# Optimization experiments

Measured on AMD Instinct MI355X. Metric: run time of the kernel, lower is better.

Reference implementation:

```python
import jax, jax.numpy as jnp
import numpy as np

V, L, H, D, S, B = 32000, 6, 16, 1024, 512, 4
DK = D // H
DF = 4 * D
EPS = 1e-5


def setup_inputs() -> dict:
    key = jax.random.key(0)
    ks = jax.random.split(key, 24)
    std = 0.02
    def w(k, shape):
        return jax.random.normal(k, shape, dtype=jnp.float32) * std
    inp = {
        'x': jax.random.randint(ks[0], (B, S), 0, V),
        'tok_emb': w(ks[1], (V, D)),
        # per-layer params stacked on leading L axis; Linear stored as [in,out]
        'wq': w(ks[2], (L, D, D)), 'bq': jnp.zeros((L, D)),
        'wk': w(ks[3], (L, D, D)), 'bk': jnp.zeros((L, D)),
        'wv': w(ks[4], (L, D, D)), 'bv': jnp.zeros((L, D)),
        'wo': w(ks[5], (L, D, D)), 'bo': jnp.zeros((L, D)),
        'ln1_g': jnp.ones((L, D)), 'ln1_b': jnp.zeros((L, D)),
        'w1': w(ks[6], (L, D, DF)), 'b1': jnp.zeros((L, DF)),
        'w2': w(ks[7], (L, DF, D)), 'b2': jnp.zeros((L, D)),
        'ln2_g': jnp.ones((L, D)), 'ln2_b': jnp.zeros((L, D)),
        'lnf_g': jnp.ones((D,)), 'lnf_b': jnp.zeros((D,)),
        'lm_w': w(ks[8], (D, V)),
    }
    return inp


def _layernorm(x, g, b):
    mu = jnp.mean(x, axis=-1, keepdims=True)
    var = jnp.mean(jnp.square(x - mu), axis=-1, keepdims=True)
    return (x - mu) * jax.lax.rsqrt(var + EPS) * g + b


def _sinusoidal_pe(seq_len, d_model):
    pos = jnp.arange(seq_len, dtype=jnp.float32)[:, None]
    div = jnp.exp(jnp.arange(0, d_model, 2, dtype=jnp.float32) * (-np.log(10000.0) / d_model))
    pe = jnp.zeros((seq_len, d_model), dtype=jnp.float32)
    pe = pe.at[:, 0::2].set(jnp.sin(pos * div))
    pe = pe.at[:, 1::2].set(jnp.cos(pos * div))
    return pe  # [S, D]


def _gpt_forward(x, tok_emb, wq, bq, wk, bk, wv, bv, wo, bo,
                 ln1_g, ln1_b, w1, b1, w2, b2, ln2_g, ln2_b,
                 lnf_g, lnf_b, lm_w):
    b, s = x.shape
    h = tok_emb[x] + _sinusoidal_pe(s, D)  # [B,S,D]
    causal = jnp.tril(jnp.ones((s, s), dtype=bool))  # True = keep
    scale = 1.0 / np.sqrt(DK)

    def block(h, p):
        (wq, bq, wk, bk, wv, bv, wo, bo,
         ln1_g, ln1_b, w1, b1, w2, b2, ln2_g, ln2_b) = p
        hn = _layernorm(h, ln1_g, ln1_b)
        q = (hn @ wq + bq).reshape(b, s, H, DK)
        k = (hn @ wk + bk).reshape(b, s, H, DK)
        v = (hn @ wv + bv).reshape(b, s, H, DK)
        scores = jnp.einsum('bqhd,bkhd->bhqk', q, k) * scale
        scores = jnp.where(causal, scores, -1e9)
        attn = jax.nn.softmax(scores, axis=-1)
        ctx = jnp.einsum('bhqk,bkhd->bqhd', attn, v).reshape(b, s, D)
        h = h + (ctx @ wo + bo)
        hn2 = _layernorm(h, ln2_g, ln2_b)
        ff = jax.nn.gelu(hn2 @ w1 + b1, approximate=False) @ w2 + b2
        return h + ff, None

    params = (wq, bq, wk, bk, wv, bv, wo, bo,
              ln1_g, ln1_b, w1, b1, w2, b2, ln2_g, ln2_b)
    h, _ = jax.lax.scan(block, h, params)
    h = _layernorm(h, lnf_g, lnf_b)
    return h @ lm_w  # [B,S,V] logits


def reference(x, tok_emb, wq, bq, wk, bk, wv, bv, wo, bo,
              ln1_g, ln1_b, w1, b1, w2, b2, ln2_g, ln2_b,
              lnf_g, lnf_b, lm_w):
    return _gpt_forward(x, tok_emb, wq, bq, wk, bk, wv, bv, wo, bo,
                        ln1_g, ln1_b, w1, b1, w2, b2, ln2_g, ln2_b,
                        lnf_g, lnf_b, lm_w)
```

## Files before the change

### kernel.cpp

```cpp
#include <hip/hip_runtime.h>
#include <hip/hip_bf16.h>
#include <math.h>

#define V_SIZE 32000
#define L_NUM 6
#define H_NUM 16
#define D_MODEL 1024
#define S_LEN 512
#define B_SZ 4
#define DF_DIM 4096
#define ROWS (B_SZ * S_LEN)
#define QKV_N (3 * D_MODEL)
#define KVBLK 64

typedef unsigned short u16;
typedef __attribute__((ext_vector_type(8))) short short8v;
typedef __attribute__((ext_vector_type(4))) float f32x4;

__device__ __forceinline__ float b2f(u16 b) {
  union { float f; unsigned u; } c; c.u = ((unsigned)b) << 16; return c.f;
}
__device__ __forceinline__ u16 f2b(float f) {
  __hip_bfloat16 h = __float2bfloat16(f);
  union { __hip_bfloat16 h; u16 u; } c; c.h = h; return c.u;
}
__device__ __forceinline__ void g2l16(const void* g, void* l) {
  __builtin_amdgcn_global_load_lds(
      (const __attribute__((address_space(1))) void*)g,
      (__attribute__((address_space(3))) void*)l, 16, 0, 0);
}

__global__ __launch_bounds__(256) void embed_kernel(
    const int* __restrict__ x, const float* __restrict__ tok_emb,
    float* __restrict__ h) {
  int row = blockIdx.x;
  int s = row % S_LEN;
  int tok = x[row];
  const float* te = tok_emb + (size_t)tok * D_MODEL;
  float* hr = h + (size_t)row * D_MODEL;
  float pos = (float)s;
  const float c = 9.210340371976184f / (float)D_MODEL;
#pragma unroll
  for (int i = 0; i < D_MODEL / 256; ++i) {
    int d = threadIdx.x + i * 256;
    float freq = expf(-(float)(d & ~1) * c);
    float ang = pos * freq;
    float pe = (d & 1) ? cosf(ang) : sinf(ang);
    hr[d] = te[d] + pe;
  }
}

__global__ __launch_bounds__(256) void layernorm_kernel(
    const float* __restrict__ in, const float* __restrict__ g,
    const float* __restrict__ b, u16* __restrict__ out) {
  const int row = blockIdx.x * 4 + (threadIdx.x >> 6);
  const int lane = threadIdx.x & 63;
  const float4* xr = (const float4*)(in + (size_t)row * D_MODEL);
  float4 v[4];
  float s1 = 0.f, s2 = 0.f;
#pragma unroll
  for (int i = 0; i < 4; ++i) {
    float4 t = xr[lane + i * 64];
    v[i] = t;
    s1 += t.x + t.y + t.z + t.w;
    s2 += t.x * t.x + t.y * t.y + t.z * t.z + t.w * t.w;
  }
#pragma unroll
  for (int off = 32; off; off >>= 1) {
    s1 += __shfl_xor(s1, off, 64);
    s2 += __shfl_xor(s2, off, 64);
  }
  const float mu = s1 * (1.0f / D_MODEL);
  const float var = s2 * (1.0f / D_MODEL) - mu * mu;
  const float rstd = rsqrtf(var + 1e-5f);
  u16* orow = out + (size_t)row * D_MODEL;
#pragma unroll
  for (int i = 0; i < 4; ++i) {
    const int d = (lane + i * 64) * 4;
    const float4 gv = *(const float4*)&g[d];
    const float4 bv = *(const float4*)&b[d];
    u16 o0 = f2b((v[i].x - mu) * rstd * gv.x + bv.x);
    u16 o1 = f2b((v[i].y - mu) * rstd * gv.y + bv.y);
    u16 o2 = f2b((v[i].z - mu) * rstd * gv.z + bv.z);
    u16 o3 = f2b((v[i].w - mu) * rstd * gv.w + bv.w);
    uint2 pk;
    pk.x = (unsigned)o0 | ((unsigned)o1 << 16);
    pk.y = (unsigned)o2 | ((unsigned)o3 << 16);
    *(uint2*)&orow[d] = pk;
  }
}

__global__ __launch_bounds__(256) void transpose_cvt(
    const float* __restrict__ W, u16* __restrict__ Wt, int K, int N,
    long out_stride) {
  __shared__ float t[64][33];
  const float* Wl = W + (size_t)blockIdx.z * K * N;
  u16* Wtl = Wt + (size_t)blockIdx.z * out_stride;
  const int n0 = blockIdx.x * 32, k0 = blockIdx.y * 64;
  const int tx = threadIdx.x & 31, ty = threadIdx.x >> 5;
#pragma unroll
  for (int i = 0; i < 64; i += 8)
    t[ty + i][tx] = Wl[(size_t)(k0 + ty + i) * N + n0 + tx];
  __syncthreads();
#pragma unroll
  for (int j = 0; j < 32; j += 8) {
    const int n = ty + j;
    u16 lo = f2b(t[2 * tx][n]);
    u16 hi = f2b(t[2 * tx + 1][n]);
    *(unsigned*)&Wtl[(size_t)(n0 + n) * K + k0 + 2 * tx] =
        (unsigned)lo | ((unsigned)hi << 16);
  }
}

__global__ __launch_bounds__(256) void pack_qkv_bias(
    const float* __restrict__ bq, const float* __restrict__ bk,
    const float* __restrict__ bv, float* __restrict__ out) {
  int i = blockIdx.x * 256 + threadIdx.x;
  int l = i / QKV_N, j = i % QKV_N;
  float v = (j < D_MODEL) ? bq[l * D_MODEL + j]
          : (j < 2 * D_MODEL) ? bk[l * D_MODEL + j - D_MODEL]
          : bv[l * D_MODEL + j - 2 * D_MODEL];
  out[i] = v;
}

template <int TM, int OUT_MODE, bool GELU_ACT, int SPLITK>
__global__ __launch_bounds__(256) void gemm_bf16(
    const u16* __restrict__ A, const u16* __restrict__ Bt,
    const float* __restrict__ bias, float* __restrict__ Cf,
    u16* __restrict__ Cb, int M, int N, int K) {
  constexpr int MF = TM / 32;
  constexpr int AINSTS = TM / 32;
  __shared__ __align__(16) u16 As[2][TM * 64];
  __shared__ __align__(16) u16 Bs[2][128 * 64];
  const int tid = threadIdx.x;
  const int wid = tid >> 6;
  const int lane = tid & 63;
  const int wr = wid >> 1, wc = wid & 1;
  const int nwg = gridDim.x;
  const int id = blockIdx.x;
  const int q = nwg >> 3, r = nwg & 7;
  const int xcd = id & 7, i0 = id >> 3;
  const int swz = (xcd < r ? xcd * (q + 1) : r * (q + 1) + (xcd - r) * q) + i0;
  const int kh = (SPLITK > 1) ? (swz & (SPLITK - 1)) : 0;
  const int rest = (SPLITK > 1) ? (swz >> 1) : swz;
  const int gm = M / TM;
  const int bm = rest % gm, bn = rest / gm;
  const int Ksub = K / SPLITK;
  const int rowi = lane >> 3;
  const int gsw = ((lane & 7) ^ rowi) * 8;
  const u16* Ag = A + (size_t)(bm * TM + wid * (TM / 4) + rowi) * K + kh * Ksub + gsw;
  const u16* Bg = Bt + (size_t)(bn * 128 + wid * 32 + rowi) * K + kh * Ksub + gsw;
  auto stage = [&](int buf, int k0) {
#pragma unroll
    for (int i = 0; i < AINSTS; ++i)
      g2l16(Ag + k0 + (size_t)(8 * i) * K, As[buf] + wid * (TM / 4) * 64 + i * 512);
#pragma unroll
    for (int i = 0; i < 4; ++i)
      g2l16(Bg + k0 + (size_t)(8 * i) * K, Bs[buf] + wid * 2048 + i * 512);
  };
  f32x4 acc[MF][4] = {};
  const int fr = lane & 15;
  const int hi = lane >> 4;
  stage(0, 0);
  __syncthreads();
  for (int k0 = 0; k0 < Ksub; k0 += 64) {
    const int cur = (k0 >> 6) & 1;
    if (k0 + 64 < Ksub) stage(cur ^ 1, k0 + 64);
    short8v a[MF][2], b[4][2];
#pragma unroll
    for (int m = 0; m < MF; ++m)
#pragma unroll
      for (int kk = 0; kk < 2; ++kk) {
        const int g = (kk * 4 + hi) ^ (fr & 7);
        a[m][kk] = *(const short8v*)&As[cur][(wr * (TM / 2) + m * 16 + fr) * 64 + g * 8];
      }
#pragma unroll
    for (int n = 0; n < 4; ++n)
#pragma unroll
      for (int kk = 0; kk < 2; ++kk) {
        const int g = (kk * 4 + hi) ^ (fr & 7);
        b[n][kk] = *(const short8v*)&Bs[cur][(wc * 64 + n * 16 + fr) * 64 + g * 8];
      }
    __builtin_amdgcn_s_setprio(1);
#pragma unroll
    for (int kk = 0; kk < 2; ++kk)
#pragma unroll
      for (int m = 0; m < MF; ++m)
#pragma unroll
        for (int n = 0; n < 4; ++n)
          acc[m][n] = __builtin_amdgcn_mfma_f32_16x16x32_bf16(a[m][kk], b[n][kk], acc[m][n], 0, 0, 0);
    __builtin_amdgcn_s_setprio(0);
    __syncthreads();
  }
  const int row0 = bm * TM + wr * (TM / 2) + hi * 4;
  const int col0 = bn * 128 + wc * 64 + fr;
#pragma unroll
  for (int m = 0; m < MF; ++m) {
#pragma unroll
    for (int n = 0; n < 4; ++n) {
      const int col = col0 + n * 16;
      float bv = (OUT_MODE == 2) ? 0.f : bias[col];
      if (SPLITK > 1 && kh != 0) bv = 0.f;
#pragma unroll
      for (int r2 = 0; r2 < 4; ++r2) {
        const int row = row0 + m * 16 + r2;
        float v = acc[m][n][r2] + bv;
        if (GELU_ACT) v = 0.5f * v * (1.0f + erff(v * 0.70710678118f));
        size_t idx = (size_t)row * N + col;
        if (OUT_MODE == 0) Cb[idx] = f2b(v);
        else if (OUT_MODE == 1) {
          if (SPLITK > 1) atomicAdd(&Cf[idx], v);
          else Cf[idx] += v;
        } else Cf[idx] = v;
      }
    }
  }
}

#define LDA_H(H)                                                            \
  _Pragma("unroll") for (int m = 0; m < 4; ++m)                             \
  _Pragma("unroll") for (int ks = 0; ks < 2; ++ks) {                        \
    const int row_ = wm * 128 + (H)*64 + m * 16 + fr;                       \
    const int g_ = (ks * 4 + hi) ^ (fr & 7);                                \
    a[m][ks] = *(const short8v*)&smem[cur * 16384 + row_ * 64 + g_ * 8];    \
  }
#define LDB_H(H)                                                            \
  _Pragma("unroll") for (int n = 0; n < 2; ++n)                             \
  _Pragma("unroll") for (int ks = 0; ks < 2; ++ks) {                        \
    const int row_ = wn * 64 + (H)*32 + n * 16 + fr;                        \
    const int g_ = (ks * 4 + hi) ^ (fr & 7);                                \
    b[n][ks] = *(const short8v*)&smem[32768 + cur * 16384 + row_ * 64 + g_ * 8]; \
  }
#define MFMA_CLUSTER(QA, QB)                                                \
  __builtin_amdgcn_s_barrier();                                             \
  asm volatile("s_waitcnt lgkmcnt(0)" ::: "memory");                        \
  __builtin_amdgcn_sched_barrier(0);                                        \
  __builtin_amdgcn_s_setprio(1);                                            \
  _Pragma("unroll") for (int ks = 0; ks < 2; ++ks)                          \
  _Pragma("unroll") for (int m = 0; m < 4; ++m)                             \
  _Pragma("unroll") for (int n = 0; n < 2; ++n)                             \
    acc[(QA)*4 + m][(QB)*2 + n] = __builtin_amdgcn_mfma_f32_16x16x32_bf16(  \
        a[m][ks], b[n][ks], acc[(QA)*4 + m][(QB)*2 + n], 0, 0, 0);          \
  __builtin_amdgcn_s_setprio(0);

__global__ __launch_bounds__(512, 2) void gemm256_lm(
    const u16* __restrict__ A, const u16* __restrict__ Bt,
    float* __restrict__ C, int M, int N, int K) {
  extern __shared__ __align__(16) u16 smem[];
  const int tid = threadIdx.x, wid = tid >> 6, lane = tid & 63;
  const int wm = wid >> 2, wn = wid & 3;
  const int fr = lane & 15, hi = lane >> 4;
  const int T = K / 64;
  const int nwg = gridDim.x, id = blockIdx.x;
  const int q = nwg >> 3, r = nwg & 7;
  const int xcd = id & 7, i0 = id >> 3;
  const int swz = (xcd < r ? xcd * (q + 1) : r * (q + 1) + (xcd - r) * q) + i0;
  const int gm = M / 256;
  const int bm = swz % gm, bn = swz / gm;
  const int rowA0 = bm * 256, rowB0 = bn * 256;
  const int rowoff = wid * 8 + (lane >> 3);
  const int gsw = ((lane & 7) ^ (lane >> 3)) * 8;
  auto stA = [&](int qq, int tt, int bb) {
    g2l16(A + (size_t)(rowA0 + qq * 64 + rowoff) * K + tt * 64 + gsw,
          smem + bb * 16384 + qq * 4096 + wid * 512);
  };
  auto stB = [&](int qq, int tt, int bb) {
    g2l16(Bt + (size_t)(rowB0 + qq * 64 + rowoff) * K + tt * 64 + gsw,
          smem + 32768 + bb * 16384 + qq * 4096 + wid * 512);
  };
  f32x4 acc[8][4] = {};
  stA(0, 0, 0); stA(2, 0, 0);
  stB(0, 0, 0); stB(1, 0, 0); stB(2, 0, 0); stB(3, 0, 0);
  stA(1, 0, 0); stA(3, 0, 0);
  if (T > 1) {
    stA(0, 1, 1); stA(2, 1, 1);
    asm volatile("s_waitcnt vmcnt(2)" ::: "memory");
  } else {
    asm volatile("s_waitcnt vmcnt(0)" ::: "memory");
  }
  __builtin_amdgcn_s_barrier();
  for (int t = 0; t < T; ++t) {
    const int cur = t & 1, nxt = cur ^ 1;
    short8v a[4][2], b[2][2];
    LDA_H(0); LDB_H(0);
    if (t + 1 < T) { stB(0, t + 1, nxt); stB(1, t + 1, nxt); }
    MFMA_CLUSTER(0, 0);
    __builtin_amdgcn_s_barrier();
    LDB_H(1);
    if (t + 1 < T) { stB(2, t + 1, nxt); stB(3, t + 1, nxt); }
    MFMA_CLUSTER(0, 1);
    __builtin_amdgcn_s_barrier();
    LDA_H(1);
    if (t + 1 < T) { stA(1, t + 1, nxt); stA(3, t + 1, nxt); }
    MFMA_CLUSTER(1, 1);
    __builtin_amdgcn_s_barrier();
    LDB_H(0);
    if (t + 2 < T) { stA(0, t + 2, cur); stA(2, t + 2, cur); }
    MFMA_CLUSTER(1, 0);
    if (t + 1 < T) {
      if (t + 2 < T) asm volatile("s_waitcnt vmcnt(2)" ::: "memory");
      else           asm volatile("s_waitcnt vmcnt(0)" ::: "memory");
      __builtin_amdgcn_s_barrier();
    }
  }
  float* lf = (float*)smem;
#pragma unroll
  for (int c = 0; c < 2; ++c) {
    __syncthreads();
    if (wm == c) {
#pragma unroll
      for (int m = 0; m < 8; ++m)
#pragma unroll
        for (int n = 0; n < 4; ++n)
#pragma unroll
          for (int rr = 0; rr < 4; ++rr)
            lf[(m * 16 + hi * 4 + rr) * 256 + wn * 64 + n * 16 + fr] =
                acc[m][n][rr];
    }
    __syncthreads();
#pragma unroll
    for (int i = 0; i < 16; ++i) {
      const int f = i * 2048 + tid * 4;
      const int rw = f >> 8, cl = f & 255;
      f32x4 v = *(const f32x4*)&lf[f];
      *(f32x4*)&C[(size_t)(rowA0 + c * 128 + rw) * N + rowB0 + cl] = v;
    }
  }
}

__global__ __launch_bounds__(256) void attn_mfma(
    const u16* __restrict__ qkv, u16* __restrict__ ctx) {
  __shared__ __align__(16) u16 smem[3 * 64 * 72];
  u16 (*Qs)[72] = (u16(*)[72])smem;
  u16 (*Ks)[72] = (u16(*)[72])(smem + 4608);
  u16 (*Vs)[72] = (u16(*)[72])(smem + 9216);
  const int qt = blockIdx.x, bh = blockIdx.y;
  const int b = bh >> 4, h = bh & 15;
  const int tid = threadIdx.x, wid = tid >> 6, lane = tid & 63;
  const int fr = lane & 15, ko = (lane >> 4) * 8;
  u16 (*Ps)[72] = (u16(*)[72])(smem + wid * 1152);
  const size_t rb = (size_t)b * S_LEN;
  const int q0 = qt * 64;
  const int hq = h * 64;
#pragma unroll
  for (int i = 0; i < 2; ++i) {
    int e = tid + i * 256, r = e >> 3, c = (e & 7) * 8;
    *(short8v*)&Qs[r][c] = *(const short8v*)&qkv[(rb + q0 + r) * QKV_N + hq + c];
  }
  __syncthreads();
  short8v qf[2];
#pragma unroll
  for (int ks = 0; ks < 2; ++ks)
    qf[ks] = *(const short8v*)&Qs[wid * 16 + fr][ks * 32 + ko];
  f32x4 acc_o[4] = {};
  float mrow[4], lrow[4];
#pragma unroll
  for (int r = 0; r < 4; ++r) { mrow[r] = -1e30f; lrow[r] = 0.f; }
  const int nt = qt + 1;
  short8v kreg[2], vreg[2];
  auto loadregs = [&](int t) {
    const int k0 = t * KVBLK;
#pragma unroll
    for (int i = 0; i < 2; ++i) {
      const int e = tid + i * 256, rr = e >> 3, cc = (e & 7) * 8;
      kreg[i] = *(const short8v*)&qkv[(rb + k0 + rr) * QKV_N + D_MODEL + hq + cc];
      vreg[i] = *(const short8v*)&qkv[(rb + k0 + rr) * QKV_N + 2 * D_MODEL + hq + cc];
    }
  };
  loadregs(0);
  for (int t = 0; t < nt; ++t) {
    __syncthreads();
#pragma unroll
    for (int i = 0; i < 2; ++i) {
      const int e = tid + i * 256, rr = e >> 3, cc = (e & 7) * 8;
      *(short8v*)&Ks[rr][cc] = kreg[i];
#pragma unroll
      for (int j = 0; j < 8; ++j) Vs[cc + j][rr] = (u16)vreg[i][j];
    }
    __syncthreads();
    if (t + 1 < nt) loadregs(t + 1);
    const int k0 = t * KVBLK;
    f32x4 s[4] = {};
    __builtin_amdgcn_s_setprio(1);
#pragma unroll
    for (int n = 0; n < 4; ++n)
#pragma unroll
      for (int ks = 0; ks < 2; ++ks) {
        short8v kf = *(const short8v*)&Ks[n * 16 + fr][ks * 32 + ko];
        s[n] = __builtin_amdgcn_mfma_f32_16x16x32_bf16(qf[ks], kf, s[n], 0, 0, 0);
      }
    __builtin_amdgcn_s_setprio(0);
    const int rbase = q0 + wid * 16 + (lane >> 4) * 4;
#pragma unroll
    for (int r = 0; r < 4; ++r) {
      const int row_g = rbase + r;
      float vmax = -1e30f;
#pragma unroll
      for (int n = 0; n < 4; ++n) {
        float v = s[n][r] * 0.125f;
        if (k0 + n * 16 + fr > row_g) v = -1e30f;
        s[n][r] = v;
        vmax = fmaxf(vmax, v);
      }
#pragma unroll
      for (int off = 1; off < 16; off <<= 1) vmax = fmaxf(vmax, __shfl_xor(vmax, off, 64));
      const float mnew = fmaxf(mrow[r], vmax);
      const float sc = expf(mrow[r] - mnew);
      mrow[r] = mnew;
      float ssum = 0.f;
#pragma unroll
      for (int n = 0; n < 4; ++n) {
        float p = expf(s[n][r] - mnew);
        s[n][r] = p;
        ssum += p;
      }
#pragma unroll
      for (int off = 1; off < 16; off <<= 1) ssum += __shfl_xor(ssum, off, 64);
      lrow[r] = lrow[r] * sc + ssum;
#pragma unroll
      for (int n = 0; n < 4; ++n) {
        acc_o[n][r] *= sc;
        Ps[(lane >> 4) * 4 + r][n * 16 + fr] = f2b(s[n][r]);
      }
    }
    __builtin_amdgcn_s_setprio(1);
#pragma unroll
    for (int ks = 0; ks < 2; ++ks) {
      short8v pf = *(const short8v*)&Ps[fr][ks * 32 + ko];
#pragma unroll
      for (int n = 0; n < 4; ++n) {
        short8v vf = *(const short8v*)&Vs[n * 16 + fr][ks * 32 + ko];
        acc_o[n] = __builtin_amdgcn_mfma_f32_16x16x32_bf16(pf, vf, acc_o[n], 0, 0, 0);
      }
    }
    __builtin_amdgcn_s_setprio(0);
  }
#pragma unroll
  for (int r = 0; r < 4; ++r) {
    const int row_g = q0 + wid * 16 + (lane >> 4) * 4 + r;
    const float inv = 1.0f / lrow[r];
#pragma unroll
    for (int n = 0; n < 4; ++n)
      ctx[(rb + row_g) * D_MODEL + hq + n * 16 + fr] = f2b(acc_o[n][r] * inv);
  }
}

extern "C" void kernel_launch(void* const* d_in, const int* in_sizes, int n_in,
                              void* d_out, int out_size, void* d_ws, size_t ws_size,
                              hipStream_t stream) {
  const int* x = (const int*)d_in[0];
  const float* tok_emb = (const float*)d_in[1];
  const float* wq = (const float*)d_in[2];
  const float* bq = (const float*)d_in[3];
  const float* wk = (const float*)d_in[4];
  const float* bk = (const float*)d_in[5];
  const float* wv = (const float*)d_in[6];
  const float* bv = (const float*)d_in[7];
  const float* wo = (const float*)d_in[8];
  const float* bo = (const float*)d_in[9];
  const float* ln1_g = (const float*)d_in[10];
  const float* ln1_b = (const float*)d_in[11];
  const float* w1 = (const float*)d_in[12];
  const float* b1 = (const float*)d_in[13];
  const float* w2 = (const float*)d_in[14];
  const float* b2 = (const float*)d_in[15];
  const float* ln2_g = (const float*)d_in[16];
  const float* ln2_b = (const float*)d_in[17];
  const float* lnf_g = (const float*)d_in[18];
  const float* lnf_b = (const float*)d_in[19];
  const float* lm_w = (const float*)d_in[20];

  char* w = (char*)d_ws;
  float* h    = (float*)(w);
  u16*  hn    = (u16*)(w + (8ll << 20));
  u16*  qkvb  = (u16*)(w + (12ll << 20));
  u16*  cbuf  = (u16*)(w + (24ll << 20));
  u16*  ff    = qkvb;
  u16*  wqkvT = (u16*)(w + (28ll << 20));
  u16*  woT   = (u16*)(w + (64ll << 20));
  u16*  w1T   = (u16*)(w + (76ll << 20));
  u16*  w2T   = (u16*)(w + (124ll << 20));
  u16*  lmT   = (u16*)(w + (172ll << 20));
  float* bqkv = (float*)(w + (235ll << 20));

  const size_t DD = (size_t)D_MODEL * D_MODEL;
  const size_t DDF = (size_t)D_MODEL * DF_DIM;
  const long QS = (long)QKV_N * D_MODEL;
  transpose_cvt<<<dim3(32, 16, L_NUM), 256, 0, stream>>>(wq, wqkvT, D_MODEL, D_MODEL, QS);
  transpose_cvt<<<dim3(32, 16, L_NUM), 256, 0, stream>>>(wk, wqkvT + DD, D_MODEL, D_MODEL, QS);
  transpose_cvt<<<dim3(32, 16, L_NUM), 256, 0, stream>>>(wv, wqkvT + 2 * DD, D_MODEL, D_MODEL, QS);
  transpose_cvt<<<dim3(32, 16, L_NUM), 256, 0, stream>>>(wo, woT, D_MODEL, D_MODEL, (long)DD);
  transpose_cvt<<<dim3(128, 16, L_NUM), 256, 0, stream>>>(w1, w1T, D_MODEL, DF_DIM, (long)DDF);
  transpose_cvt<<<dim3(32, 64, L_NUM), 256, 0, stream>>>(w2, w2T, DF_DIM, D_MODEL, (long)DDF);
  transpose_cvt<<<dim3(V_SIZE / 32, 16, 1), 256, 0, stream>>>(lm_w, lmT, D_MODEL, V_SIZE, 0);
  pack_qkv_bias<<<L_NUM * QKV_N / 256, 256, 0, stream>>>(bq, bk, bv, bqkv);

  embed_kernel<<<ROWS, 256, 0, stream>>>(x, tok_emb, h);

  const int nQKV = (ROWS / 64) * (QKV_N / 128);
  const int nPRJ = 2 * (ROWS / 64) * (D_MODEL / 128);
  const int nFF1 = (ROWS / 64) * (DF_DIM / 128);
  const int nFF2 = 2 * (ROWS / 64) * (D_MODEL / 128);
  for (int l = 0; l < L_NUM; ++l) {
    layernorm_kernel<<<ROWS / 4, 256, 0, stream>>>(h, ln1_g + l * D_MODEL, ln1_b + l * D_MODEL, hn);
    gemm_bf16<64, 0, false, 1><<<nQKV, 256, 0, stream>>>(
        hn, wqkvT + (size_t)l * QS, bqkv + l * QKV_N, nullptr, qkvb,
        ROWS, QKV_N, D_MODEL);
    attn_mfma<<<dim3(S_LEN / 64, B_SZ * H_NUM), 256, 0, stream>>>(qkvb, cbuf);
    gemm_bf16<64, 1, false, 2><<<nPRJ, 256, 0, stream>>>(
        cbuf, woT + l * DD, bo + l * D_MODEL, h, nullptr, ROWS, D_MODEL, D_MODEL);
    layernorm_kernel<<<ROWS / 4, 256, 0, stream>>>(h, ln2_g + l * D_MODEL, ln2_b + l * D_MODEL, hn);
    gemm_bf16<64, 0, true, 1><<<nFF1, 256, 0, stream>>>(
        hn, w1T + l * DDF, b1 + l * DF_DIM, nullptr, ff, ROWS, DF_DIM, D_MODEL);
    gemm_bf16<64, 1, false, 2><<<nFF2, 256, 0, stream>>>(
        ff, w2T + l * DDF, b2 + l * D_MODEL, h, nullptr, ROWS, D_MODEL, DF_DIM);
  }
  layernorm_kernel<<<ROWS / 4, 256, 0, stream>>>(h, lnf_g, lnf_b, hn);

  hipFuncSetAttribute((const void*)gemm256_lm,
                      hipFuncAttributeMaxDynamicSharedMemorySize, 131072);
  const int nLM = (ROWS / 256) * (V_SIZE / 256);
  gemm256_lm<<<nLM, 512, 131072, stream>>>(
      hn, lmT, (float*)d_out, ROWS, V_SIZE, D_MODEL);
}
```

Baseline: 1.412 ms.

## Split causal attention KV range into chunks with separate combine kernel

Attention is split into 12 jobs per (batch, head), so query tiles 4-7 process their KV blocks in two chunks of at most four blocks each. Partial unnormalized outputs and row max/sum go to workspace in fp32, and a new combine kernel merges them with log-sum-exp rescaling and writes bf16 context. This evens out the causal workload imbalance and raises block count, at the cost of an extra launch and fp32 intermediate traffic. The LM-head GEMM output store is also switched to nontemporal stores.

```diff
diff --git a/kernel.cpp b/kernel.cpp
--- a/kernel.cpp
+++ b/kernel.cpp
@@ -12,6 +12,7 @@
 #define ROWS (B_SZ * S_LEN)
 #define QKV_N (3 * D_MODEL)
 #define KVBLK 64
+#define NJOB 12
 
 typedef unsigned short u16;
 typedef __attribute__((ext_vector_type(8))) short short8v;
@@ -323,18 +324,23 @@
       const int f = i * 2048 + tid * 4;
       const int rw = f >> 8, cl = f & 255;
       f32x4 v = *(const f32x4*)&lf[f];
-      *(f32x4*)&C[(size_t)(rowA0 + c * 128 + rw) * N + rowB0 + cl] = v;
-    }
-  }
-}
-
-__global__ __launch_bounds__(256) void attn_mfma(
-    const u16* __restrict__ qkv, u16* __restrict__ ctx) {
+      __builtin_nontemporal_store(
+          v, (f32x4*)&C[(size_t)(rowA0 + c * 128 + rw) * N + rowB0 + cl]);
+    }
+  }
+}
+
+__global__ __launch_bounds__(256) void attn_part(
+    const u16* __restrict__ qkv, float* __restrict__ Op,
+    float* __restrict__ Ml) {
   __shared__ __align__(16) u16 smem[3 * 64 * 72];
   u16 (*Qs)[72] = (u16(*)[72])smem;
   u16 (*Ks)[72] = (u16(*)[72])(smem + 4608);
   u16 (*Vs)[72] = (u16(*)[72])(smem + 9216);
-  const int qt = blockIdx.x, bh = blockIdx.y;
+  const int job = blockIdx.x, bh = blockIdx.y;
+  constexpr int qt_of[NJOB] = {0, 1, 2, 3, 4, 4, 5, 5, 6, 6, 7, 7};
+  constexpr int ch_of[NJOB] = {0, 0, 0, 0, 0, 1, 0, 1, 0, 1, 0, 1};
+  const int qt = qt_of[job], ch = ch_of[job];
   const int b = bh >> 4, h = bh & 15;
   const int tid = threadIdx.x, wid = tid >> 6, lane = tid & 63;
   const int fr = lane & 15, ko = (lane >> 4) * 8;
@@ -342,6 +348,8 @@
   const size_t rb = (size_t)b * S_LEN;
   const int q0 = qt * 64;
   const int hq = h * 64;
+  const int t_lo = ch * 4;
+  const int t_hi = (qt + 1 < t_lo + 4) ? qt + 1 : t_lo + 4;
 #pragma unroll
   for (int i = 0; i < 2; ++i) {
     int e = tid + i * 256, r = e >> 3, c = (e & 7) * 8;
@@ -356,7 +364,6 @@
   float mrow[4], lrow[4];
 #pragma unroll
   for (int r = 0; r < 4; ++r) { mrow[r] = -1e30f; lrow[r] = 0.f; }
-  const int nt = qt + 1;
   short8v kreg[2], vreg[2];
   auto loadregs = [&](int t) {
     const int k0 = t * KVBLK;
@@ -367,8 +374,8 @@
       vreg[i] = *(const short8v*)&qkv[(rb + k0 + rr) * QKV_N + 2 * D_MODEL + hq + cc];
     }
   };
-  loadregs(0);
-  for (int t = 0; t < nt; ++t) {
+  loadregs(t_lo);
+  for (int t = t_lo; t < t_hi; ++t) {
     __syncthreads();
 #pragma unroll
     for (int i = 0; i < 2; ++i) {
@@ -378,7 +385,7 @@
       for (int j = 0; j < 8; ++j) Vs[cc + j][rr] = (u16)vreg[i][j];
     }
     __syncthreads();
-    if (t + 1 < nt) loadregs(t + 1);
+    if (t + 1 < t_hi) loadregs(t + 1);
     const int k0 = t * KVBLK;
     f32x4 s[4] = {};
     __builtin_amdgcn_s_setprio(1);
@@ -435,13 +442,57 @@
     }
     __builtin_amdgcn_s_setprio(0);
   }
+  const size_t jb = (size_t)(bh * NJOB + job);
 #pragma unroll
   for (int r = 0; r < 4; ++r) {
-    const int row_g = q0 + wid * 16 + (lane >> 4) * 4 + r;
-    const float inv = 1.0f / lrow[r];
-#pragma unroll
-    for (int n = 0; n < 4; ++n)
-      ctx[(rb + row_g) * D_MODEL + hq + n * 16 + fr] = f2b(acc_o[n][r] * inv);
+    const int row_l = wid * 16 + (lane >> 4) * 4 + r;
+    const size_t base = (jb * 64 + row_l) * 64;
+#pragma unroll
+    for (int n = 0; n < 4; ++n) Op[base + n * 16 + fr] = acc_o[n][r];
+    if (fr == 0) {
+      Ml[jb * 128 + row_l * 2] = mrow[r];
+      Ml[jb * 128 + row_l * 2 + 1] = lrow[r];
+    }
+  }
+}
+
+__global__ __launch_bounds__(256) void attn_combine(
+    const float* __restrict__ Op, const float* __restrict__ Ml,
+    u16* __restrict__ ctx) {
+  const int qt = blockIdx.x, bh = blockIdx.y;
+  const int b = bh >> 4, h = bh & 15;
+  constexpr int job0_of[8] = {0, 1, 2, 3, 4, 6, 8, 10};
+  const int j0 = job0_of[qt];
+  const bool two = qt >= 4;
+  const size_t rb = (size_t)b * S_LEN;
+  const int q0 = qt * 64, hq = h * 64;
+  const size_t jb1 = (size_t)(bh * NJOB + j0);
+  const size_t jb2 = jb1 + 1;
+#pragma unroll
+  for (int i = 0; i < 4; ++i) {
+    const int idx4 = threadIdx.x + i * 256;
+    const int row = idx4 >> 4, c4 = (idx4 & 15) * 4;
+    f32x4 o1 = *(const f32x4*)&Op[(jb1 * 64 + row) * 64 + c4];
+    const float m1 = Ml[jb1 * 128 + row * 2], l1 = Ml[jb1 * 128 + row * 2 + 1];
+    float o[4];
+    float inv;
+    if (two) {
+      f32x4 o2 = *(const f32x4*)&Op[(jb2 * 64 + row) * 64 + c4];
+      const float m2 = Ml[jb2 * 128 + row * 2], l2 = Ml[jb2 * 128 + row * 2 + 1];
+      const float m = fmaxf(m1, m2);
+      const float e1 = expf(m1 - m), e2 = expf(m2 - m);
+      inv = 1.0f / (l1 * e1 + l2 * e2);
+#pragma unroll
+      for (int j = 0; j < 4; ++j) o[j] = o1[j] * e1 + o2[j] * e2;
+    } else {
+      inv = 1.0f / l1;
+#pragma unroll
+      for (int j = 0; j < 4; ++j) o[j] = o1[j];
+    }
+    uint2 pk;
+    pk.x = (unsigned)f2b(o[0] * inv) | ((unsigned)f2b(o[1] * inv) << 16);
+    pk.y = (unsigned)f2b(o[2] * inv) | ((unsigned)f2b(o[3] * inv) << 16);
+    *(uint2*)&ctx[(rb + q0 + row) * D_MODEL + hq + c4] = pk;
   }
 }
 
@@ -482,6 +533,8 @@
   u16*  w2T   = (u16*)(w + (124ll << 20));
   u16*  lmT   = (u16*)(w + (172ll << 20));
   float* bqkv = (float*)(w + (235ll << 20));
+  float* Op   = (float*)(w + (236ll << 20));
+  float* Ml   = (float*)(w + (249ll << 20));
 
   const size_t DD = (size_t)D_MODEL * D_MODEL;
   const size_t DDF = (size_t)D_MODEL * DF_DIM;
@@ -506,7 +559,8 @@
     gemm_bf16<64, 0, false, 1><<<nQKV, 256, 0, stream>>>(
         hn, wqkvT + (size_t)l * QS, bqkv + l * QKV_N, nullptr, qkvb,
         ROWS, QKV_N, D_MODEL);
-    attn_mfma<<<dim3(S_LEN / 64, B_SZ * H_NUM), 256, 0, stream>>>(qkvb, cbuf);
+    attn_part<<<dim3(NJOB, B_SZ * H_NUM), 256, 0, stream>>>(qkvb, Op, Ml);
+    attn_combine<<<dim3(S_LEN / 64, B_SZ * H_NUM), 256, 0, stream>>>(Op, Ml, cbuf);
     gemm_bf16<64, 1, false, 2><<<nPRJ, 256, 0, stream>>>(
         cbuf, woT + l * DD, bo + l * D_MODEL, h, nullptr, ROWS, D_MODEL, D_MODEL);
     layernorm_kernel<<<ROWS / 4, 256, 0, stream>>>(h, ln2_g + l * D_MODEL, ln2_b + l * D_MODEL, hn);
```

Measured after the change: 1.373 ms. 2.8% less time.
